# Kernel tuning notes

Hardware: AMD Instinct MI355X
Metric: run time of the kernel (lower is better)

Reference implementation:

```python
import jax, jax.numpy as jnp
import numpy as np

NUM_HEADS = 16
D_MODEL = 1024
D_K = D_MODEL // NUM_HEADS


def setup_inputs() -> dict:
    key = jax.random.key(0)
    ks = jax.random.split(key, 11)
    B, S = 2, 2048
    s = 1.0 / np.sqrt(D_MODEL)
    return {
        "Q": jax.random.normal(ks[0], (B, S, D_MODEL), jnp.float32),
        "K": jax.random.normal(ks[1], (B, S, D_MODEL), jnp.float32),
        "V": jax.random.normal(ks[2], (B, S, D_MODEL), jnp.float32),
        "Wq": jax.random.normal(ks[3], (D_MODEL, D_MODEL), jnp.float32) * s,
        "bq": jnp.zeros((D_MODEL,), jnp.float32),
        "Wk": jax.random.normal(ks[4], (D_MODEL, D_MODEL), jnp.float32) * s,
        "bk": jnp.zeros((D_MODEL,), jnp.float32),
        "Wv": jax.random.normal(ks[5], (D_MODEL, D_MODEL), jnp.float32) * s,
        "bv": jnp.zeros((D_MODEL,), jnp.float32),
        "Wo": jax.random.normal(ks[6], (D_MODEL, D_MODEL), jnp.float32) * s,
        "bo": jnp.zeros((D_MODEL,), jnp.float32),
    }


def _split_heads(x):
    B, S, _ = x.shape
    return x.reshape(B, S, NUM_HEADS, D_K).transpose(0, 2, 1, 3)  # (B,H,S,Dk)


def reference(Q, K, V, Wq, bq, Wk, bk, Wv, bv, Wo, bo):
    q = _split_heads(Q @ Wq + bq)
    k = _split_heads(K @ Wk + bk)
    v = _split_heads(V @ Wv + bv)
    scores = jnp.einsum("bhqd,bhkd->bhqk", q, k) / jnp.sqrt(jnp.asarray(D_K, q.dtype))
    attn = jax.nn.softmax(scores, axis=-1)
    out = jnp.einsum("bhqk,bhkd->bhqd", attn, v)  # (B,H,S,Dk)
    B, H, S, Dk = out.shape
    combined = out.transpose(0, 2, 1, 3).reshape(B, S, H * Dk)
    return combined @ Wo + bo
```

## Files before the change

### kernel.cpp

```cpp
#include <hip/hip_runtime.h>
#include <stdint.h>

#define DM   1024
#define NH   16
#define DKH  64
#define SEQ  2048
#define NB   2

typedef __attribute__((ext_vector_type(8))) short  frag8;
typedef __attribute__((ext_vector_type(4))) short  frag4;
typedef __attribute__((ext_vector_type(4))) short  short4v;
typedef __attribute__((ext_vector_type(8))) short  short8v;
typedef __attribute__((ext_vector_type(4))) float  f32x4;

__device__ __forceinline__ unsigned short f2bf(float x){
  unsigned u = __float_as_uint(x);
  u += 0x7fffu + ((u >> 16) & 1u);
  return (unsigned short)(u >> 16);
}

#define GLOAD16(GP, LP) __builtin_amdgcn_global_load_lds( \
    (__attribute__((address_space(1))) void*)(GP), \
    (__attribute__((address_space(3))) void*)(LP), 16, 0, 0)


__global__ __launch_bounds__(256) void cast_qkv(const float* __restrict__ Q,
                                                const float* __restrict__ K,
                                                const float* __restrict__ V,
                                                short* __restrict__ dst){
  const int z = blockIdx.z;
  const float* src = (z == 0) ? Q : (z == 1 ? K : V);
  const int i = (blockIdx.x * 256 + threadIdx.x) * 4;
  float4 f = *(const float4*)(src + i);
  short4v s;
  s.x = (short)f2bf(f.x); s.y = (short)f2bf(f.y);
  s.z = (short)f2bf(f.z); s.w = (short)f2bf(f.w);
  *(short4v*)(dst + (long)z * (SEQ*NB*DM) + i) = s;
}

__global__ __launch_bounds__(256) void wtrans(const float* __restrict__ Wq,
                                              const float* __restrict__ Wk,
                                              const float* __restrict__ Wv,
                                              const float* __restrict__ Wo,
                                              short* __restrict__ wt){
  const int z = blockIdx.z;
  const float* W = (z == 0) ? Wq : (z == 1 ? Wk : (z == 2 ? Wv : Wo));
  short* out = wt + (long)z * (DM*DM);
  __shared__ float t[32][33];
  const int n0 = blockIdx.x * 32, k0 = blockIdx.y * 32;
  const int c = threadIdx.x & 31, r0 = threadIdx.x >> 5;
#pragma unroll
  for (int i = 0; i < 4; ++i){
    int r = r0 + i * 8;
    t[r][c] = W[(k0 + r) * DM + n0 + c];
  }
  __syncthreads();
#pragma unroll
  for (int i = 0; i < 4; ++i){
    int r = r0 + i * 8;
    out[(n0 + r) * DM + k0 + c] = (short)f2bf(t[c][r]);
  }
}

__device__ __forceinline__ void store_out(short* p, float v){ *p = (short)f2bf(v); }
__device__ __forceinline__ void store_out(float* p, float v){ *p = v; }

template<typename OT>
__global__ __launch_bounds__(256) void gemm_bt(const short* __restrict__ Abase, long Astride,
                                               const short* __restrict__ Btbase, long Btstride,
                                               const float* __restrict__ bias0,
                                               const float* __restrict__ bias1,
                                               const float* __restrict__ bias2,
                                               OT* __restrict__ Cbase, long Cstride,
                                               float qscale){
  const int z = blockIdx.z;
  const short* A  = Abase + (long)z * Astride;
  const short* Bt = Btbase + (long)z * Btstride;
  OT* C = Cbase + (long)z * Cstride;
  const float* bias = (z == 0) ? bias0 : (z == 1 ? bias1 : bias2);
  const float scale = (z == 0) ? qscale : 1.0f;
  const int KD = DM, ND = DM;

  __shared__ __align__(16) short As[128 * 64];
  __shared__ __align__(16) short Bs[128 * 64];

  const int tid = threadIdx.x;
  const int w = tid >> 6, lane = tid & 63, l15 = lane & 15, quad = lane >> 4;
  const int wy = w >> 1, wx = w & 1;
  const int bm = blockIdx.x * 128, bn = blockIdx.y * 128;
  const int lrow = lane >> 3;
  const int lcolsw = (((lane & 7) ^ lrow) & 7) * 8;

  f32x4 acc[4][4] = {};

  for (int kt = 0; kt < KD; kt += 64){
#pragma unroll
    for (int i = 0; i < 4; ++i){
      int j = w * 4 + i;
      GLOAD16(A  + (bm + j * 8 + lrow) * KD + kt + lcolsw, &As[j * 512]);
      GLOAD16(Bt + (bn + j * 8 + lrow) * KD + kt + lcolsw, &Bs[j * 512]);
    }
    __syncthreads();
#pragma unroll
    for (int ks = 0; ks < 2; ++ks){
      frag8 af[4], bf_[4];
#pragma unroll
      for (int mt = 0; mt < 4; ++mt)
        af[mt] = *(const frag8*)&As[(wy * 64 + mt * 16 + l15) * 64 +
                                    (((ks * 4 + quad) ^ (l15 & 7)) * 8)];
#pragma unroll
      for (int nt = 0; nt < 4; ++nt)
        bf_[nt] = *(const frag8*)&Bs[(wx * 64 + nt * 16 + l15) * 64 +
                                     (((ks * 4 + quad) ^ (l15 & 7)) * 8)];
#pragma unroll
      for (int mt = 0; mt < 4; ++mt)
#pragma unroll
        for (int nt = 0; nt < 4; ++nt)
          acc[mt][nt] = __builtin_amdgcn_mfma_f32_16x16x32_bf16(af[mt], bf_[nt], acc[mt][nt], 0, 0, 0);
    }
    __syncthreads();
  }

#pragma unroll
  for (int mt = 0; mt < 4; ++mt){
#pragma unroll
    for (int r = 0; r < 4; ++r){
      int m = bm + wy * 64 + mt * 16 + quad * 4 + r;
#pragma unroll
      for (int nt = 0; nt < 4; ++nt){
        int n = bn + wx * 64 + nt * 16 + l15;
        float v = (acc[mt][nt][r] + bias[n]) * scale;
        store_out(&C[(long)m * ND + n], v);
      }
    }
  }
}

template<typename OT>
__global__ __launch_bounds__(256) void gemm64_bt(const short* __restrict__ A,
                                                 const short* __restrict__ Bt,
                                                 const float* __restrict__ bias,
                                                 OT* __restrict__ C,
                                                 float scale){
  const int KD = DM, ND = DM;
  __shared__ __align__(16) short As[64 * 64];
  __shared__ __align__(16) short Bs[128 * 64];
  const int tid = threadIdx.x;
  const int w = tid >> 6, lane = tid & 63, l15 = lane & 15, quad = lane >> 4;
  const int wy = w >> 1, wx = w & 1;
  const int bm = blockIdx.x * 64, bn = blockIdx.y * 128;
  const int lrow = lane >> 3;
  const int lcolsw = (((lane & 7) ^ lrow) & 7) * 8;
  f32x4 acc[2][4] = {};

  for (int kt = 0; kt < KD; kt += 64){
#pragma unroll
    for (int i = 0; i < 2; ++i){
      int j = w * 2 + i;
      GLOAD16(A + (bm + j * 8 + lrow) * KD + kt + lcolsw, &As[j * 512]);
    }
#pragma unroll
    for (int i = 0; i < 4; ++i){
      int j = w * 4 + i;
      GLOAD16(Bt + (bn + j * 8 + lrow) * KD + kt + lcolsw, &Bs[j * 512]);
    }
    __syncthreads();
#pragma unroll
    for (int ks = 0; ks < 2; ++ks){
      frag8 af[2], bf_[4];
#pragma unroll
      for (int mt = 0; mt < 2; ++mt)
        af[mt] = *(const frag8*)&As[(wy * 32 + mt * 16 + l15) * 64 +
                                    (((ks * 4 + quad) ^ (l15 & 7)) * 8)];
#pragma unroll
      for (int nt = 0; nt < 4; ++nt)
        bf_[nt] = *(const frag8*)&Bs[(wx * 64 + nt * 16 + l15) * 64 +
                                     (((ks * 4 + quad) ^ (l15 & 7)) * 8)];
#pragma unroll
      for (int mt = 0; mt < 2; ++mt)
#pragma unroll
        for (int nt = 0; nt < 4; ++nt)
          acc[mt][nt] = __builtin_amdgcn_mfma_f32_16x16x32_bf16(af[mt], bf_[nt], acc[mt][nt], 0, 0, 0);
    }
    __syncthreads();
  }

#pragma unroll
  for (int mt = 0; mt < 2; ++mt){
#pragma unroll
    for (int r = 0; r < 4; ++r){
      int m = bm + wy * 32 + mt * 16 + quad * 4 + r;
#pragma unroll
      for (int nt = 0; nt < 4; ++nt){
        int n = bn + wx * 64 + nt * 16 + l15;
        store_out(&C[(long)m * ND + n], (acc[mt][nt][r] + bias[n]) * scale);
      }
    }
  }
}

__global__ __launch_bounds__(256) void vtrans(const short* __restrict__ v,
                                              short* __restrict__ vt){
  const int bh = blockIdx.y;
  const int b = bh >> 4, h = bh & 15;
  const int s0 = blockIdx.x * 64;
  __shared__ short tT[64][66];
  const short* vb = v + ((long)(b * SEQ + s0)) * DM + h * DKH;
  for (int j = threadIdx.x; j < 512; j += 256){
    int row = j >> 3, off = (j & 7) * 8;
    short8v d = *(const short8v*)(vb + row * DM + off);
#pragma unroll
    for (int e = 0; e < 8; ++e) tT[off + e][row] = d[e];
  }
  __syncthreads();
  short* out = vt + (long)bh * (DKH * SEQ) + s0;
  for (int j = threadIdx.x; j < 512; j += 256){
    int dr = j >> 3, soff = (j & 7) * 8;
    short8v o;
#pragma unroll
    for (int e = 0; e < 8; ++e) o[e] = tT[dr][soff + e];
    *(short8v*)(out + dr * SEQ + soff) = o;
  }
}

__global__ __launch_bounds__(256) void flash(const short* __restrict__ q,
                                             const short* __restrict__ k,
                                             const short* __restrict__ vt,
                                             short* __restrict__ comb){
  const int bh = blockIdx.y;
  const int b = bh >> 4, h = bh & 15;
  const int q0 = blockIdx.x * 64;
  const int tid = threadIdx.x;
  const int w = tid >> 6, lane = tid & 63, l15 = lane & 15, quad = lane >> 4;

  __shared__ __align__(16) short Ks[64 * 64];
  __shared__ __align__(16) short Vs[64 * 64];

  frag8 aq[2];
  const short* qb = q + ((long)(b * SEQ + q0 + w * 16)) * DM + h * DKH;
#pragma unroll
  for (int ks = 0; ks < 2; ++ks)
    aq[ks] = *(const frag8*)(qb + l15 * DM + ks * 32 + quad * 8);

  frag4 ones4;
#pragma unroll
  for (int e = 0; e < 4; ++e) ones4[e] = (short)0x3F80;

  f32x4 O[4] = {};
  f32x4 Lacc = {0.f, 0.f, 0.f, 0.f};

  const short* kb  = k + ((long)b * SEQ) * DM + h * DKH;
  const short* vtb = vt + (long)bh * (DKH * SEQ);
  const int lrow8 = lane >> 3;
  const int lcolsw = (((lane & 7) ^ lrow8) & 7) * 8;

  for (int kt = 0; kt < SEQ / 64; ++kt){
#pragma unroll
    for (int i = 0; i < 2; ++i){
      int jj = w * 2 + i;
      GLOAD16(kb + (kt * 64 + jj * 8 + lrow8) * DM + lcolsw, &Ks[jj * 512]);
      GLOAD16(vtb + (jj * 8 + lrow8) * SEQ + kt * 64 + lcolsw, &Vs[jj * 512]);
    }
    __syncthreads();

    f32x4 scT[4];
#pragma unroll
    for (int nt = 0; nt < 4; ++nt) scT[nt] = (f32x4){0.f, 0.f, 0.f, 0.f};
#pragma unroll
    for (int ks = 0; ks < 2; ++ks){
#pragma unroll
      for (int nt = 0; nt < 4; ++nt){
        frag8 ak = *(const frag8*)&Ks[(nt * 16 + l15) * 64 +
                                      (((ks * 4 + quad) ^ (l15 & 7)) * 8)];
        scT[nt] = __builtin_amdgcn_mfma_f32_16x16x32_bf16(ak, aq[ks], scT[nt], 0, 0, 0);
      }
    }

    frag4 ap[4];
#pragma unroll
    for (int nt = 0; nt < 4; ++nt){
#pragma unroll
      for (int r = 0; r < 4; ++r){
        unsigned u = (__float_as_uint(__expf(scT[nt][r])) + 0x8000u) >> 16;
        ap[nt][r] = (short)u;
      }
    }

#pragma unroll
    for (int nt = 0; nt < 4; ++nt){
#pragma unroll
      for (int dt = 0; dt < 4; ++dt){
        frag4 bv4 = *(const frag4*)&Vs[(dt * 16 + l15) * 64 +
                                       (((nt * 2 + (quad >> 1)) ^ (l15 & 7)) * 8) +
                                       (quad & 1) * 4];
        O[dt] = __builtin_amdgcn_mfma_f32_16x16x16bf16_1k(ap[nt], bv4, O[dt], 0, 0, 0);
      }
      Lacc = __builtin_amdgcn_mfma_f32_16x16x16bf16_1k(ap[nt], ones4, Lacc, 0, 0, 0);
    }
    __syncthreads();
  }

  short* ob = comb + ((long)(b * SEQ + q0 + w * 16)) * DM + h * DKH;
#pragma unroll
  for (int r = 0; r < 4; ++r){
    float inv = 1.f / Lacc[r];
#pragma unroll
    for (int nt = 0; nt < 4; ++nt)
      ob[(quad * 4 + r) * DM + nt * 16 + l15] = (short)f2bf(O[nt][r] * inv);
  }
}

extern "C" void kernel_launch(void* const* d_in, const int* in_sizes, int n_in,
                              void* d_out, int out_size, void* d_ws, size_t ws_size,
                              hipStream_t stream){
  const float* Q  = (const float*)d_in[0];
  const float* K  = (const float*)d_in[1];
  const float* V  = (const float*)d_in[2];
  const float* Wq = (const float*)d_in[3];
  const float* bq = (const float*)d_in[4];
  const float* Wk = (const float*)d_in[5];
  const float* bk = (const float*)d_in[6];
  const float* Wv = (const float*)d_in[7];
  const float* bv = (const float*)d_in[8];
  const float* Wo = (const float*)d_in[9];
  const float* bo = (const float*)d_in[10];
  float* out = (float*)d_out;

  const long TEN = (long)NB * SEQ * DM;
  const long WEL = (long)DM * DM;
  short* ws   = (short*)d_ws;
  short* xc   = ws;
  short* wt   = xc + 3 * TEN;
  short* qkv  = wt + 4 * WEL;
  short* vtr  = qkv + 3 * TEN;
  short* comb = vtr + TEN;

  cast_qkv<<<dim3(4096, 1, 3), 256, 0, stream>>>(Q, K, V, xc);
  wtrans<<<dim3(32, 32, 4), 256, 0, stream>>>(Wq, Wk, Wv, Wo, wt);
  gemm_bt<short><<<dim3(32, 8, 3), 256, 0, stream>>>(xc, TEN, wt, WEL, bq, bk, bv,
                                                     qkv, TEN, 0.125f);
  vtrans<<<dim3(32, 32), 256, 0, stream>>>(qkv + 2 * TEN, vtr);
  flash<<<dim3(32, 32), 256, 0, stream>>>(qkv, qkv + TEN, vtr, comb);
  gemm64_bt<float><<<dim3(64, 8), 256, 0, stream>>>(comb, wt + 3 * WEL, bo, out, 1.0f);
  (void)in_sizes; (void)n_in; (void)out_size; (void)ws_size;
}
```

Measured before the change: 248.3 us.

## Use exp2 with log2e-folded Q scale and repack V tile for 128-bit LDS reads

The Q projection scale now carries a log2(e) factor so the flash kernel can use the hardware exp2 builtin instead of __expf, dropping a multiply per element. The V tile is loaded into LDS with 4-byte global_load_lds transfers through a permuted address map, so each lane can read one 8-short fragment and split it across two MFMAs instead of doing two 4-short LDS reads. This trades more, smaller global-to-LDS loads for fewer LDS read instructions, and the new index math risks coalescing loss or layout errors.

```diff
diff --git a/kernel.cpp b/kernel.cpp
--- a/kernel.cpp
+++ b/kernel.cpp
@@ -19,9 +19,16 @@
   return (unsigned short)(u >> 16);
 }
 
+__device__ __forceinline__ float dev_exp2(float x){
+  return __builtin_amdgcn_exp2f(x);
+}
+
 #define GLOAD16(GP, LP) __builtin_amdgcn_global_load_lds( \
     (__attribute__((address_space(1))) void*)(GP), \
     (__attribute__((address_space(3))) void*)(LP), 16, 0, 0)
+#define GLOAD4(GP, LP) __builtin_amdgcn_global_load_lds( \
+    (__attribute__((address_space(1))) void*)(GP), \
+    (__attribute__((address_space(3))) void*)(LP), 4, 0, 0)
 
 
 __global__ __launch_bounds__(256) void cast_qkv(const float* __restrict__ Q,
@@ -254,13 +261,33 @@
   const int lrow8 = lane >> 3;
   const int lcolsw = (((lane & 7) ^ lrow8) & 7) * 8;
 
+  const short* vsrc[8];
+  short* vdst[8];
+  {
+    const int P = lane & 31, Bb = P >> 2, t = (P >> 1) & 1, u = P & 1;
+    const int rhalf = lane >> 5;
+#pragma unroll
+    for (int i = 0; i < 8; ++i){
+      int pair = w * 8 + i;
+      int row  = pair * 2 + rhalf;
+      int blk0 = (Bb - (row & 7)) & 7;
+      int qd = blk0 >> 1, ch = blk0 & 1;
+      int nt = ch * 2 + t;
+      int Ldw = nt * 8 + qd * 2 + u;
+      vsrc[i] = vtb + (long)row * SEQ + Ldw * 2;
+      vdst[i] = &Vs[pair * 128];
+    }
+  }
+
   for (int kt = 0; kt < SEQ / 64; ++kt){
 #pragma unroll
     for (int i = 0; i < 2; ++i){
       int jj = w * 2 + i;
       GLOAD16(kb + (kt * 64 + jj * 8 + lrow8) * DM + lcolsw, &Ks[jj * 512]);
-      GLOAD16(vtb + (jj * 8 + lrow8) * SEQ + kt * 64 + lcolsw, &Vs[jj * 512]);
-    }
+    }
+#pragma unroll
+    for (int i = 0; i < 8; ++i)
+      GLOAD4(vsrc[i] + kt * 64, vdst[i]);
     __syncthreads();
 
     f32x4 scT[4];
@@ -279,23 +306,27 @@
     frag4 ap[4];
 #pragma unroll
     for (int nt = 0; nt < 4; ++nt){
-#pragma unroll
-      for (int r = 0; r < 4; ++r){
-        unsigned u = (__float_as_uint(__expf(scT[nt][r])) + 0x8000u) >> 16;
-        ap[nt][r] = (short)u;
+      float e0 = dev_exp2(scT[nt][0]), e1 = dev_exp2(scT[nt][1]);
+      float e2 = dev_exp2(scT[nt][2]), e3 = dev_exp2(scT[nt][3]);
+      ap[nt][0] = (short)((__float_as_uint(e0) + 0x8000u) >> 16);
+      ap[nt][1] = (short)((__float_as_uint(e1) + 0x8000u) >> 16);
+      ap[nt][2] = (short)((__float_as_uint(e2) + 0x8000u) >> 16);
+      ap[nt][3] = (short)((__float_as_uint(e3) + 0x8000u) >> 16);
+    }
+
+#pragma unroll
+    for (int ch = 0; ch < 2; ++ch){
+#pragma unroll
+      for (int dt = 0; dt < 4; ++dt){
+        frag8 vv = *(const frag8*)&Vs[(dt * 16 + l15) * 64 +
+                                      (((quad * 2 + ch + (l15 & 7)) & 7) * 8)];
+        frag4 b0 = __builtin_shufflevector(vv, vv, 0, 1, 2, 3);
+        frag4 b1 = __builtin_shufflevector(vv, vv, 4, 5, 6, 7);
+        O[dt] = __builtin_amdgcn_mfma_f32_16x16x16bf16_1k(ap[ch * 2],     b0, O[dt], 0, 0, 0);
+        O[dt] = __builtin_amdgcn_mfma_f32_16x16x16bf16_1k(ap[ch * 2 + 1], b1, O[dt], 0, 0, 0);
       }
-    }
-
-#pragma unroll
-    for (int nt = 0; nt < 4; ++nt){
-#pragma unroll
-      for (int dt = 0; dt < 4; ++dt){
-        frag4 bv4 = *(const frag4*)&Vs[(dt * 16 + l15) * 64 +
-                                       (((nt * 2 + (quad >> 1)) ^ (l15 & 7)) * 8) +
-                                       (quad & 1) * 4];
-        O[dt] = __builtin_amdgcn_mfma_f32_16x16x16bf16_1k(ap[nt], bv4, O[dt], 0, 0, 0);
-      }
-      Lacc = __builtin_amdgcn_mfma_f32_16x16x16bf16_1k(ap[nt], ones4, Lacc, 0, 0, 0);
+      Lacc = __builtin_amdgcn_mfma_f32_16x16x16bf16_1k(ap[ch * 2],     ones4, Lacc, 0, 0, 0);
+      Lacc = __builtin_amdgcn_mfma_f32_16x16x16bf16_1k(ap[ch * 2 + 1], ones4, Lacc, 0, 0, 0);
     }
     __syncthreads();
   }
@@ -338,7 +369,7 @@
   cast_qkv<<<dim3(4096, 1, 3), 256, 0, stream>>>(Q, K, V, xc);
   wtrans<<<dim3(32, 32, 4), 256, 0, stream>>>(Wq, Wk, Wv, Wo, wt);
   gemm_bt<short><<<dim3(32, 8, 3), 256, 0, stream>>>(xc, TEN, wt, WEL, bq, bk, bv,
-                                                     qkv, TEN, 0.125f);
+                                                     qkv, TEN, 0.125f * 1.44269504f);
   vtrans<<<dim3(32, 32), 256, 0, stream>>>(qkv + 2 * TEN, vtr);
   flash<<<dim3(32, 32), 256, 0, stream>>>(qkv, qkv + TEN, vtr, comb);
   gemm64_bt<float><<<dim3(64, 8), 256, 0, stream>>>(comb, wt + 3 * WEL, bo, out, 1.0f);
```

New measurement: 244.7 us. No clear change (-1.4%).

## Process 128 queries per flash block and fold log2e into Q scaling for exp2

Applied to the files above, without the earlier changes.

Each wave of the flash kernel now handles two 16-row query tiles (128 queries per block), so every K/V tile loaded into LDS and every K fragment read feeds twice as many MFMAs, halving K/V global traffic. The softmax exponent switches from __expf to the hardware exp2 intrinsic, with log2(e) folded into the Q projection scale. The costs are higher register pressure from doubled accumulators and half as many blocks (512), which may lower occupancy and load balance.

```diff
diff --git a/kernel.cpp b/kernel.cpp
--- a/kernel.cpp
+++ b/kernel.cpp
@@ -17,6 +17,10 @@
   unsigned u = __float_as_uint(x);
   u += 0x7fffu + ((u >> 16) & 1u);
   return (unsigned short)(u >> 16);
+}
+
+__device__ __forceinline__ float dev_exp2(float x){
+  return __builtin_amdgcn_exp2f(x);
 }
 
 #define GLOAD16(GP, LP) __builtin_amdgcn_global_load_lds( \
@@ -229,25 +233,27 @@
                                              short* __restrict__ comb){
   const int bh = blockIdx.y;
   const int b = bh >> 4, h = bh & 15;
-  const int q0 = blockIdx.x * 64;
+  const int q0 = blockIdx.x * 128;
   const int tid = threadIdx.x;
   const int w = tid >> 6, lane = tid & 63, l15 = lane & 15, quad = lane >> 4;
 
   __shared__ __align__(16) short Ks[64 * 64];
   __shared__ __align__(16) short Vs[64 * 64];
 
-  frag8 aq[2];
-  const short* qb = q + ((long)(b * SEQ + q0 + w * 16)) * DM + h * DKH;
-#pragma unroll
-  for (int ks = 0; ks < 2; ++ks)
-    aq[ks] = *(const frag8*)(qb + l15 * DM + ks * 32 + quad * 8);
+  frag8 aq[2][2];
+  const short* qb = q + ((long)(b * SEQ + q0 + w * 32)) * DM + h * DKH;
+#pragma unroll
+  for (int mt = 0; mt < 2; ++mt)
+#pragma unroll
+    for (int ks = 0; ks < 2; ++ks)
+      aq[mt][ks] = *(const frag8*)(qb + (mt * 16 + l15) * DM + ks * 32 + quad * 8);
 
   frag4 ones4;
 #pragma unroll
   for (int e = 0; e < 4; ++e) ones4[e] = (short)0x3F80;
 
-  f32x4 O[4] = {};
-  f32x4 Lacc = {0.f, 0.f, 0.f, 0.f};
+  f32x4 O[2][4] = {};
+  f32x4 Lacc[2] = {{0.f,0.f,0.f,0.f},{0.f,0.f,0.f,0.f}};
 
   const short* kb  = k + ((long)b * SEQ) * DM + h * DKH;
   const short* vtb = vt + (long)bh * (DKH * SEQ);
@@ -263,28 +269,34 @@
     }
     __syncthreads();
 
-    f32x4 scT[4];
-#pragma unroll
-    for (int nt = 0; nt < 4; ++nt) scT[nt] = (f32x4){0.f, 0.f, 0.f, 0.f};
+    f32x4 scT[2][4];
+#pragma unroll
+    for (int mt = 0; mt < 2; ++mt)
+#pragma unroll
+      for (int nt = 0; nt < 4; ++nt) scT[mt][nt] = (f32x4){0.f, 0.f, 0.f, 0.f};
 #pragma unroll
     for (int ks = 0; ks < 2; ++ks){
 #pragma unroll
       for (int nt = 0; nt < 4; ++nt){
         frag8 ak = *(const frag8*)&Ks[(nt * 16 + l15) * 64 +
                                       (((ks * 4 + quad) ^ (l15 & 7)) * 8)];
-        scT[nt] = __builtin_amdgcn_mfma_f32_16x16x32_bf16(ak, aq[ks], scT[nt], 0, 0, 0);
-      }
-    }
-
-    frag4 ap[4];
-#pragma unroll
-    for (int nt = 0; nt < 4; ++nt){
-#pragma unroll
-      for (int r = 0; r < 4; ++r){
-        unsigned u = (__float_as_uint(__expf(scT[nt][r])) + 0x8000u) >> 16;
-        ap[nt][r] = (short)u;
-      }
-    }
+#pragma unroll
+        for (int mt = 0; mt < 2; ++mt)
+          scT[mt][nt] = __builtin_amdgcn_mfma_f32_16x16x32_bf16(ak, aq[mt][ks], scT[mt][nt], 0, 0, 0);
+      }
+    }
+
+    frag4 ap[2][4];
+#pragma unroll
+    for (int mt = 0; mt < 2; ++mt)
+#pragma unroll
+      for (int nt = 0; nt < 4; ++nt){
+#pragma unroll
+        for (int r = 0; r < 4; ++r){
+          float e = dev_exp2(scT[mt][nt][r]);
+          ap[mt][nt][r] = (short)((__float_as_uint(e) + 0x8000u) >> 16);
+        }
+      }
 
 #pragma unroll
     for (int nt = 0; nt < 4; ++nt){
@@ -293,20 +305,27 @@
         frag4 bv4 = *(const frag4*)&Vs[(dt * 16 + l15) * 64 +
                                        (((nt * 2 + (quad >> 1)) ^ (l15 & 7)) * 8) +
                                        (quad & 1) * 4];
-        O[dt] = __builtin_amdgcn_mfma_f32_16x16x16bf16_1k(ap[nt], bv4, O[dt], 0, 0, 0);
-      }
-      Lacc = __builtin_amdgcn_mfma_f32_16x16x16bf16_1k(ap[nt], ones4, Lacc, 0, 0, 0);
-    }
-    __syncthreads();
-  }
-
-  short* ob = comb + ((long)(b * SEQ + q0 + w * 16)) * DM + h * DKH;
-#pragma unroll
-  for (int r = 0; r < 4; ++r){
-    float inv = 1.f / Lacc[r];
-#pragma unroll
-    for (int nt = 0; nt < 4; ++nt)
-      ob[(quad * 4 + r) * DM + nt * 16 + l15] = (short)f2bf(O[nt][r] * inv);
+#pragma unroll
+        for (int mt = 0; mt < 2; ++mt)
+          O[mt][dt] = __builtin_amdgcn_mfma_f32_16x16x16bf16_1k(ap[mt][nt], bv4, O[mt][dt], 0, 0, 0);
+      }
+#pragma unroll
+      for (int mt = 0; mt < 2; ++mt)
+        Lacc[mt] = __builtin_amdgcn_mfma_f32_16x16x16bf16_1k(ap[mt][nt], ones4, Lacc[mt], 0, 0, 0);
+    }
+    __syncthreads();
+  }
+
+  short* ob = comb + ((long)(b * SEQ + q0 + w * 32)) * DM + h * DKH;
+#pragma unroll
+  for (int mt = 0; mt < 2; ++mt){
+#pragma unroll
+    for (int r = 0; r < 4; ++r){
+      float inv = 1.f / Lacc[mt][r];
+#pragma unroll
+      for (int nt = 0; nt < 4; ++nt)
+        ob[(mt * 16 + quad * 4 + r) * DM + nt * 16 + l15] = (short)f2bf(O[mt][nt][r] * inv);
+    }
   }
 }
 
@@ -338,9 +357,9 @@
   cast_qkv<<<dim3(4096, 1, 3), 256, 0, stream>>>(Q, K, V, xc);
   wtrans<<<dim3(32, 32, 4), 256, 0, stream>>>(Wq, Wk, Wv, Wo, wt);
   gemm_bt<short><<<dim3(32, 8, 3), 256, 0, stream>>>(xc, TEN, wt, WEL, bq, bk, bv,
-                                                     qkv, TEN, 0.125f);
+                                                     qkv, TEN, 0.125f * 1.44269504f);
   vtrans<<<dim3(32, 32), 256, 0, stream>>>(qkv + 2 * TEN, vtr);
-  flash<<<dim3(32, 32), 256, 0, stream>>>(qkv, qkv + TEN, vtr, comb);
+  flash<<<dim3(16, 32), 256, 0, stream>>>(qkv, qkv + TEN, vtr, comb);
   gemm64_bt<float><<<dim3(64, 8), 256, 0, stream>>>(comb, wt + 3 * WEL, bo, out, 1.0f);
   (void)in_sizes; (void)n_in; (void)out_size; (void)ws_size;
 }
```

New measurement: 244.0 us. Within noise of the previous version (-1.7%).
